# Optimization experiments

Measured on AMD Instinct MI355X. Metric: run time of the kernel, lower is better.

Reference implementation:

```python
import jax, jax.numpy as jnp
import numpy as np

NEG = -1e30  # safe 'log zero' for fp32 (avoids -inf NaNs in grads)


def _ctc_loss(logits, targets, input_lengths, target_lengths):
    """PyTorch-semantics CTC loss: blank=0, reduction='mean', zero_infinity=True.
    logits: [B,T,C] (pre-log-softmax), targets: [B,S] padded, lengths: [B].
    """
    B, T, C = logits.shape
    S = targets.shape[1]
    L = 2 * S + 1  # extended target length (blanks interleaved)
    logp = jax.nn.log_softmax(logits, axis=-1)  # [B,T,C]

    # extended targets: blank, y1, blank, y2, ..., blank
    ext = jnp.zeros((B, L), jnp.int32).at[:, 1::2].set(targets.astype(jnp.int32))
    lp_ext = jnp.take_along_axis(
        logp, jnp.broadcast_to(ext[:, None, :], (B, T, L)), axis=2)  # [B,T,L]

    pos = jnp.arange(L)
    ext_m2 = jnp.pad(ext, ((0, 0), (2, 0)))[:, :L]
    can_skip = (ext != 0) & (ext != ext_m2) & (pos >= 2)  # [B,L]

    def shift(a, k):
        return jnp.pad(a, ((0, 0), (k, 0)), constant_values=NEG)[:, :L]

    def lse3(a, b, c):
        m = jnp.maximum(jnp.maximum(a, b), c)
        return m + jnp.log(jnp.exp(a - m) + jnp.exp(b - m) + jnp.exp(c - m))

    alpha0 = (jnp.full((B, L), NEG, logits.dtype)
              .at[:, 0].set(lp_ext[:, 0, 0])
              .at[:, 1].set(lp_ext[:, 0, 1]))

    def step(alpha, xs):
        lp_t, t = xs  # lp_t: [B,L]
        a2 = shift(alpha, 1)
        a3 = jnp.where(can_skip, shift(alpha, 2), NEG)
        new = lp_t + lse3(alpha, a2, a3)
        # freeze alpha once past each sample's input_length
        alpha = jnp.where((t < input_lengths)[:, None], new, alpha)
        return alpha, None

    lp_T = jnp.swapaxes(lp_ext, 0, 1)  # [T,B,L]
    alpha, _ = jax.lax.scan(step, alpha0, (lp_T[1:], jnp.arange(1, T)))

    i1 = (2 * target_lengths - 1).astype(jnp.int32)
    i2 = (2 * target_lengths).astype(jnp.int32)
    a_last = jnp.take_along_axis(alpha, i1[:, None], axis=1)[:, 0]
    a_blank = jnp.take_along_axis(alpha, i2[:, None], axis=1)[:, 0]
    loss = -jnp.logaddexp(a_last, a_blank)  # [B]
    loss = jnp.where(loss > 1e29, 0.0, loss)  # zero_infinity=True
    return jnp.mean(loss / target_lengths.astype(loss.dtype))


def setup_inputs() -> dict:
    key = jax.random.key(0)
    ks = jax.random.split(key, 8)
    B, T = 32, 2000
    C_err, S_err = 4, 50
    C_ph, S_ph = 64, 200
    error_logits = jax.random.normal(ks[0], (B, T, C_err), jnp.float32)
    phoneme_logits = jax.random.normal(ks[1], (B, T, C_ph), jnp.float32)
    # labels in [1, C): blank=0 never appears in targets
    error_targets = jax.random.randint(ks[2], (B, S_err), 1, C_err, jnp.int32)
    phoneme_targets = jax.random.randint(ks[3], (B, S_ph), 1, C_ph, jnp.int32)
    error_input_lengths = jax.random.randint(ks[4], (B,), T - T // 4, T + 1, jnp.int32)
    phoneme_input_lengths = jax.random.randint(ks[5], (B,), T - T // 4, T + 1, jnp.int32)
    error_target_lengths = jax.random.randint(ks[6], (B,), S_err // 2, S_err + 1, jnp.int32)
    phoneme_target_lengths = jax.random.randint(ks[7], (B,), S_ph // 2, S_ph + 1, jnp.int32)
    return {
        "error_logits": error_logits,
        "phoneme_logits": phoneme_logits,
        "error_targets": error_targets,
        "phoneme_targets": phoneme_targets,
        "error_input_lengths": error_input_lengths,
        "phoneme_input_lengths": phoneme_input_lengths,
        "error_target_lengths": error_target_lengths,
        "phoneme_target_lengths": phoneme_target_lengths,
    }


def reference(error_logits, phoneme_logits, error_targets, phoneme_targets,
              error_input_lengths, phoneme_input_lengths,
              error_target_lengths, phoneme_target_lengths):
    error_weight = 1.0
    phoneme_weight = 1.0
    error_loss = _ctc_loss(error_logits, error_targets,
                           error_input_lengths, error_target_lengths)
    phoneme_loss = _ctc_loss(phoneme_logits, phoneme_targets,
                             phoneme_input_lengths, phoneme_target_lengths)
    total_loss = error_weight * error_loss + phoneme_weight * phoneme_loss
    return total_loss
```

## Files before the change

### kernel.cpp

```cpp
#include <hip/hip_runtime.h>
#include <math.h>


static constexpr float  LOG2E = 1.4426950408889634f;
static constexpr double LN2D  = 0.6931471805599453;
static constexpr int GROWS = 2032;

#define DPP_WAVE_SHR1   0x138
#define DPP_ROW_SHR(n)  (0x110 | (n))
#define DPP_ROW_BCAST15 0x142
#define DPP_ROW_BCAST31 0x143

__device__ __forceinline__ float fexp2(float x) {
  return __builtin_amdgcn_exp2f(x);
}
__device__ __forceinline__ float flog2(float x) {
  return __builtin_amdgcn_logf(x);
}

__device__ __forceinline__ double dpp_shr1_f64(double x) {
  int lo = __double2loint(x), hi = __double2hiint(x);
  lo = __builtin_amdgcn_update_dpp(0, lo, DPP_WAVE_SHR1, 0xf, 0xf, true);
  hi = __builtin_amdgcn_update_dpp(0, hi, DPP_WAVE_SHR1, 0xf, 0xf, true);
  return __hiloint2double(hi, lo);
}

__device__ __forceinline__ int imax2(int a, int b) { return a > b ? a : b; }

__device__ __forceinline__ int wave_imax(int v) {
  v = imax2(v, __builtin_amdgcn_update_dpp(0, v, DPP_ROW_SHR(1), 0xf, 0xf, true));
  v = imax2(v, __builtin_amdgcn_update_dpp(0, v, DPP_ROW_SHR(2), 0xf, 0xf, true));
  v = imax2(v, __builtin_amdgcn_update_dpp(0, v, DPP_ROW_SHR(4), 0xf, 0xf, true));
  v = imax2(v, __builtin_amdgcn_update_dpp(0, v, DPP_ROW_SHR(8), 0xf, 0xf, true));
  v = imax2(v, __builtin_amdgcn_update_dpp(0, v, DPP_ROW_BCAST15, 0xf, 0xf, true));
  v = imax2(v, __builtin_amdgcn_update_dpp(0, v, DPP_ROW_BCAST31, 0xf, 0xf, true));
  return __builtin_amdgcn_readlane(v, 63);
}

template <int SZ>
__device__ __forceinline__ void dma(const float* g, float* l) {
  auto gp = (const __attribute__((address_space(1))) void*)g;
  auto lp = (__attribute__((address_space(3))) void*)l;
  if constexpr (SZ == 4) {
    __builtin_amdgcn_global_load_lds(gp, lp, 4, 0, 0);
  } else {
    __builtin_amdgcn_global_load_lds(gp, lp, 16, 0, 0);
  }
}

__device__ __forceinline__ void wait_vmcnt16() {
  __builtin_amdgcn_sched_barrier(0);
  __builtin_amdgcn_s_waitcnt(20336);
  __builtin_amdgcn_sched_barrier(0);
}
__device__ __forceinline__ void wait_vmcnt0() {
  __builtin_amdgcn_sched_barrier(0);
  __builtin_amdgcn_s_waitcnt(3952);
  __builtin_amdgcn_sched_barrier(0);
}


__global__ __launch_bounds__(256) void gather_all_kernel(
    const float* __restrict__ ph_logits, const float* __restrict__ err_logits,
    const int* __restrict__ ph_tgt, const int* __restrict__ err_tgt,
    float* __restrict__ Gph, float* __restrict__ Ger,
    float* __restrict__ Lpb_ph, float* __restrict__ Lpb_er) {
  const int lane = threadIdx.x & 63;
  const int t = blockIdx.x * 4 + (threadIdx.x >> 6);
  const int b = blockIdx.y;
  if (blockIdx.z == 0) {
    const float z = ph_logits[((size_t)b * 2000 + t) * 64 + lane] * LOG2E;
    float m = z;
#pragma unroll
    for (int off = 32; off >= 1; off >>= 1) m = fmaxf(m, __shfl_xor(m, off, 64));
    const float zm = z - m;
    const float e = fexp2(zm);
    float s = e;
#pragma unroll
    for (int off = 32; off >= 1; off >>= 1) s += __shfl_xor(s, off, 64);
    const int ei = __float_as_int(e);
    const float e0 = __int_as_float(__builtin_amdgcn_readlane(ei, 0));
    const float inv0 = 1.0f / e0;
    const int* tb = ph_tgt + b * 200;
    float o[4];
#pragma unroll
    for (int k = 0; k < 4; ++k) {
      const int si = lane * 4 + k;
      const int cls = (si < 200) ? tb[si] : 0;
      const float v = __int_as_float(__builtin_amdgcn_ds_bpermute(cls << 2, ei));
      o[k] = (si < 200) ? (v * inv0) : 0.0f;
    }
    *(float4*)(Gph + ((size_t)b * GROWS + t) * 256 + lane * 4) =
        make_float4(o[0], o[1], o[2], o[3]);
    if (lane == 0)
      Lpb_ph[(size_t)b * GROWS + t] = zm - flog2(s);
  } else {
    const float4 v = *(const float4*)(err_logits + ((size_t)b * 2000 + t) * 4);
    const float z0 = v.x * LOG2E, z1 = v.y * LOG2E, z2 = v.z * LOG2E,
                z3 = v.w * LOG2E;
    const float m = fmaxf(fmaxf(z0, z1), fmaxf(z2, z3));
    const float e0 = fexp2(z0 - m), e1 = fexp2(z1 - m);
    const float e2 = fexp2(z2 - m), e3 = fexp2(z3 - m);
    const int c1 = err_tgt[b * 50 + (lane < 50 ? lane : 49)];
    const float num = (c1 == 1) ? e1 : (c1 == 2) ? e2 : e3;
    Ger[((size_t)b * GROWS + t) * 64 + lane] = (lane < 50) ? (num / e0) : 0.0f;
    if (lane == 0)
      Lpb_er[(size_t)b * GROWS + t] = (z0 - m) - flog2(e0 + e1 + e2 + e3);
  }
}

template <int P> struct RowP { float v[P]; };

template <int P>
__device__ __forceinline__ RowP<P> load_rowp(const float* p) {
  RowP<P> r;
  if constexpr (P == 4) {
    const float4 a = *(const float4*)p;
    r.v[0] = a.x; r.v[1] = a.y; r.v[2] = a.z; r.v[3] = a.w;
  } else {
    r.v[0] = *p;
  }
  return r;
}

template <int P>
__device__ __forceinline__ void bl_renorm(double (&B)[P], double (&L)[P],
                                          int& K) {
  double mm = B[0];
#pragma unroll
  for (int k = 0; k < P; ++k) mm = fmax(fmax(mm, B[k]), L[k]);
  const int ex = (__double2hiint(mm) >> 20) & 0x7ff;
  const int emax = wave_imax(ex);
  if (emax > 0) {
    int d = 1523 - emax;
    if (d > 1023) d = 1023;
    if (d < -1022) d = -1022;
    const double sc = __hiloint2double((d + 1023) << 20, 0);
#pragma unroll
    for (int k = 0; k < P; ++k) { B[k] *= sc; L[k] *= sc; }
    K += d;
  }
}

template <int P>
__device__ __forceinline__ void bl_step(double (&B)[P], double (&L)[P],
                                        const double (&skipm)[P],
                                        const RowP<P>& f) {
  const double Lm1 = dpp_shr1_f64(L[P - 1]);
  double nB[P], nL[P];
#pragma unroll
  for (int k = 0; k < P; ++k) {
    const double Lp = (k >= 1) ? L[k - 1] : Lm1;
    nB[k] = B[k] + Lp;
    nL[k] = (double)f.v[k] * fma(skipm[k], Lp, B[k] + L[k]);
  }
#pragma unroll
  for (int k = 0; k < P; ++k) { B[k] = nB[k]; L[k] = nL[k]; }
}

template <int P, int S>
__device__ __forceinline__ void chain_bl3(
    const float* __restrict__ Glab,
    const float* __restrict__ Lpb,
    const int* __restrict__ tb, int len, int tl,
    float* __restrict__ out, double* sa, float* stage) {
  constexpr int LSTRIDE = 64 * P;
  const int lane = threadIdx.x;

  float spb = 0.f;
  for (int t = lane; t < len; t += 64) spb += Lpb[t];
#pragma unroll
  for (int off = 32; off >= 1; off >>= 1) spb += __shfl_xor(spb, off, 64);

  double skipm[P];
#pragma unroll
  for (int k = 0; k < P; ++k) {
    const int s = lane * P + k;
    skipm[k] = (s >= 1 && s < S && tb[s] != tb[s - 1]) ? 1.0 : 0.0;
  }

  double B[P], L[P];
#pragma unroll
  for (int k = 0; k < P; ++k) { B[k] = 0.0; L[k] = 0.0; }
  {
    const float r0 = Glab[0];
    if (lane == 0) { B[0] = 1.0; L[0] = (double)r0; }
  }
  int K = 0;

  const int ngroups = (len - 1) / 16;
  auto issue_group = [&](int g, int buf) {
    const float* rb = Glab + (size_t)(1 + g * 16) * LSTRIDE + lane * P;
    float* lb = stage + (size_t)buf * 16 * LSTRIDE;
#pragma unroll
    for (int u = 0; u < 16; ++u)
      dma<P * 4>(rb + u * LSTRIDE, lb + u * LSTRIDE);
  };

  if (ngroups >= 1) issue_group(0, 0);
  if (ngroups >= 2) issue_group(1, 1);

  for (int g = 0; g < ngroups; ++g) {
    if (g + 1 < ngroups) wait_vmcnt16();
    else                 wait_vmcnt0();
    bl_renorm<P>(B, L, K);
    const float* lb = stage + (size_t)(g & 1) * 16 * LSTRIDE + lane * P;
    RowP<P> c0 = load_rowp<P>(lb);
    RowP<P> c1 = load_rowp<P>(lb + LSTRIDE);
#pragma unroll
    for (int u = 0; u < 16; ++u) {
      RowP<P> c2 = c1;
      if (u + 2 < 16) c2 = load_rowp<P>(lb + (u + 2) * LSTRIDE);
      bl_step<P>(B, L, skipm, c0);
      c0 = c1; c1 = c2;
    }
    if (g + 2 < ngroups) issue_group(g + 2, g & 1);
  }
  for (int t = 1 + ngroups * 16; t < len; ++t) {
    if (((t - 1) & 15) == 0) bl_renorm<P>(B, L, K);
    const RowP<P> f = load_rowp<P>(Glab + (size_t)t * LSTRIDE + lane * P);
    bl_step<P>(B, L, skipm, f);
  }

  double* saB = sa;
  double* saL = sa + 64 * P;
#pragma unroll
  for (int k = 0; k < P; ++k) {
    saB[lane * P + k] = B[k];
    saL[lane * P + k] = L[k];
  }
  __syncthreads();
  if (lane == 0) {
    const double a = saL[tl - 1] + saB[tl];
    float loss = (float)((double)K * LN2D - log(a) - (double)spb * LN2D);
    if (!(loss < 1e29f)) loss = 0.f;
    atomicAdd(out, loss / ((float)tl * 32.0f));
  }
}

__global__ __launch_bounds__(64) void ctc_chains_dma_kernel(
    const float* __restrict__ Gph, const float* __restrict__ Ger,
    const float* __restrict__ Lpb_ph, const float* __restrict__ Lpb_er,
    const int* __restrict__ err_tgt, const int* __restrict__ ph_tgt,
    const int* __restrict__ err_il, const int* __restrict__ ph_il,
    const int* __restrict__ err_tl, const int* __restrict__ ph_tl,
    float* __restrict__ out) {
  __shared__ float stage[2 * 16 * 256];
  __shared__ double sa[512];
  const int blk = blockIdx.x;
  if (blk < 32) {
    int len = err_il[blk]; if (len > 2000) len = 2000;
    chain_bl3<1, 50>(Ger + (size_t)blk * GROWS * 64,
                     Lpb_er + (size_t)blk * GROWS, err_tgt + blk * 50, len,
                     err_tl[blk], out, sa, stage);
  } else {
    const int b = blk - 32;
    int len = ph_il[b]; if (len > 2000) len = 2000;
    chain_bl3<4, 200>(Gph + (size_t)b * GROWS * 256,
                      Lpb_ph + (size_t)b * GROWS, ph_tgt + b * 200, len,
                      ph_tl[b], out, sa, stage);
  }
}


__global__ __launch_bounds__(256) void softmax4_kernel(
    const float* __restrict__ x, float* __restrict__ p, int nrows) {
  int r = blockIdx.x * blockDim.x + threadIdx.x;
  if (r >= nrows) return;
  float4 v = *reinterpret_cast<const float4*>(x + (size_t)r * 4);
  float z0 = v.x * LOG2E, z1 = v.y * LOG2E, z2 = v.z * LOG2E, z3 = v.w * LOG2E;
  float m = fmaxf(fmaxf(z0, z1), fmaxf(z2, z3));
  float e0 = fexp2(z0 - m), e1 = fexp2(z1 - m);
  float e2 = fexp2(z2 - m), e3 = fexp2(z3 - m);
  float inv = 1.0f / (e0 + e1 + e2 + e3);
  float4 o;
  o.x = e0 * inv; o.y = e1 * inv; o.z = e2 * inv; o.w = e3 * inv;
  *reinterpret_cast<float4*>(p + (size_t)r * 4) = o;
}

__global__ __launch_bounds__(256) void softmax64_kernel(
    const float* __restrict__ x, float* __restrict__ p, int nrows) {
  int row = blockIdx.x * 4 + (threadIdx.x >> 6);
  int lane = threadIdx.x & 63;
  if (row >= nrows) return;
  float z = x[(size_t)row * 64 + lane] * LOG2E;
  float m = z;
#pragma unroll
  for (int off = 32; off >= 1; off >>= 1) m = fmaxf(m, __shfl_xor(m, off, 64));
  float e = fexp2(z - m);
  float s = e;
#pragma unroll
  for (int off = 32; off >= 1; off >>= 1) s += __shfl_xor(s, off, 64);
  p[(size_t)row * 64 + lane] = e * (1.0f / s);
}

template <int C, int S, int R>
__device__ __forceinline__ void ctc_chain_lin_fb(
    const float* __restrict__ p_b, const int* __restrict__ tgt_b,
    int len, int tl, float* __restrict__ out, double* sa) {
  constexpr int L = 2 * S + 1;
  const int lane = threadIdx.x;
  int idx[R];
  double skipm[R];
#pragma unroll
  for (int j = 0; j < R; ++j) {
    const int l = lane * R + j;
    int cls = 0;
    bool sk = false;
    if (l & 1) {
      const int s = (l - 1) >> 1;
      const int sc = (s < S) ? s : (S - 1);
      cls = tgt_b[sc];
      if (s >= 1 && s < S) sk = (cls != tgt_b[s - 1]);
    }
    idx[j] = cls * 4;
    skipm[j] = sk ? 1.0 : 0.0;
  }
  double alpha[R];
#pragma unroll
  for (int j = 0; j < R; ++j) {
    const int l = lane * R + j;
    alpha[j] = (l <= 1) ? (double)p_b[idx[j] >> 2] : 0.0;
  }
  int K = 0;
  const int cl = lane & (C - 1);
  float rv = p_b[(size_t)((1 < len - 1) ? 1 : (len - 1)) * C + cl];
  float pf[R];
#pragma unroll
  for (int j = 0; j < R; ++j)
    pf[j] = __int_as_float(__builtin_amdgcn_ds_bpermute(idx[j], __float_as_int(rv)));
  rv = p_b[(size_t)((2 < len - 1) ? 2 : (len - 1)) * C + cl];
  for (int t = 1; t < len; ++t) {
    if ((t & 31) == 0) {
      double m = alpha[0];
#pragma unroll
      for (int j = 1; j < R; ++j) m = fmax(m, alpha[j]);
#pragma unroll
      for (int off = 1; off < 64; off <<= 1) m = fmax(m, __shfl_xor(m, off, 64));
      const long long bits = __double_as_longlong(m);
      const int e = (int)((bits >> 52) & 0x7FF);
      if (e > 0) {
        const double sc = __longlong_as_double((long long)(2046 - e) << 52);
#pragma unroll
        for (int j = 0; j < R; ++j) alpha[j] *= sc;
        K += 1023 - e;
      }
    }
    const int tn = (t + 2 < len) ? (t + 2) : (len - 1);
    const float rvn = p_b[(size_t)tn * C + cl];
    float pfn[R];
#pragma unroll
    for (int j = 0; j < R; ++j)
      pfn[j] = __int_as_float(__builtin_amdgcn_ds_bpermute(idx[j], __float_as_int(rv)));
    double am1 = __shfl_up(alpha[R - 1], 1, 64);
    double am2 = __shfl_up(alpha[R - 2], 1, 64);
    if (lane == 0) { am1 = 0.0; am2 = 0.0; }
    double na[R];
#pragma unroll
    for (int j = 0; j < R; ++j) {
      const double a0 = alpha[j];
      const double a1 = (j >= 1) ? alpha[j - 1] : am1;
      const double a2 = (j >= 2) ? alpha[j - 2] : ((j == 1) ? am1 : am2);
      double s = a0 + a1;
      s = fma(skipm[j], a2, s);
      na[j] = (double)pf[j] * s;
    }
#pragma unroll
    for (int j = 0; j < R; ++j) alpha[j] = na[j];
#pragma unroll
    for (int j = 0; j < R; ++j) pf[j] = pfn[j];
    rv = rvn;
  }
#pragma unroll
  for (int j = 0; j < R; ++j) {
    const int l = lane * R + j;
    if (l < L) sa[l] = alpha[j];
  }
  __syncthreads();
  if (lane == 0) {
    const double a = sa[2 * tl - 1] + sa[2 * tl];
    float loss = (float)((double)K * LN2D - log(a));
    if (!(loss < 1e29f)) loss = 0.0f;
    atomicAdd(out, loss / ((float)tl * 32.0f));
  }
}

__global__ __launch_bounds__(64) void ctc_chains_fb_kernel(
    const float* __restrict__ p_err, const float* __restrict__ p_ph,
    const int* __restrict__ err_tgt, const int* __restrict__ ph_tgt,
    const int* __restrict__ err_il, const int* __restrict__ ph_il,
    const int* __restrict__ err_tl, const int* __restrict__ ph_tl,
    float* __restrict__ out) {
  __shared__ double sa[512];
  const int T = 2000;
  const int blk = blockIdx.x;
  if (blk < 32) {
    const int b = blk;
    int len = err_il[b]; if (len > T) len = T;
    ctc_chain_lin_fb<4, 50, 2>(p_err + (size_t)b * T * 4, err_tgt + b * 50, len,
                               err_tl[b], out, sa);
  } else {
    const int b = blk - 32;
    int len = ph_il[b]; if (len > T) len = T;
    ctc_chain_lin_fb<64, 200, 7>(p_ph + (size_t)b * T * 64, ph_tgt + b * 200,
                                 len, ph_tl[b], out, sa);
  }
}


extern "C" void kernel_launch(void* const* d_in, const int* in_sizes, int n_in,
                              void* d_out, int out_size, void* d_ws,
                              size_t ws_size, hipStream_t stream) {
  const float* err_logits = (const float*)d_in[0];
  const float* ph_logits  = (const float*)d_in[1];
  const int* err_tgt = (const int*)d_in[2];
  const int* ph_tgt  = (const int*)d_in[3];
  const int* err_il  = (const int*)d_in[4];
  const int* ph_il   = (const int*)d_in[5];
  const int* err_tl  = (const int*)d_in[6];
  const int* ph_tl   = (const int*)d_in[7];
  float* out = (float*)d_out;

  const size_t gph = (size_t)32 * GROWS * 256;
  const size_t ger = (size_t)32 * GROWS * 64;
  const size_t lpb = (size_t)32 * GROWS;
  const size_t need = (gph + ger + 2 * lpb) * sizeof(float);

  (void)hipMemsetAsync(d_out, 0, sizeof(float), stream);

  if (ws_size >= need) {
    float* Gph = (float*)d_ws;
    float* Ger = Gph + gph;
    float* Lpb_ph = Ger + ger;
    float* Lpb_er = Lpb_ph + lpb;
    dim3 grid(500, 32, 2);
    gather_all_kernel<<<grid, 256, 0, stream>>>(ph_logits, err_logits, ph_tgt,
                                                err_tgt, Gph, Ger, Lpb_ph,
                                                Lpb_er);
    ctc_chains_dma_kernel<<<64, 64, 0, stream>>>(Gph, Ger, Lpb_ph, Lpb_er,
                                                 err_tgt, ph_tgt, err_il,
                                                 ph_il, err_tl, ph_tl, out);
  } else {
    const int B = 32, T = 2000;
    const int rows = B * T;
    float* p_err = (float*)d_ws;
    float* p_ph  = p_err + (size_t)rows * 4;
    softmax4_kernel<<<(rows + 255) / 256, 256, 0, stream>>>(err_logits, p_err, rows);
    softmax64_kernel<<<(rows + 3) / 4, 256, 0, stream>>>(ph_logits, p_ph, rows);
    ctc_chains_fb_kernel<<<64, 64, 0, stream>>>(p_err, p_ph, err_tgt, ph_tgt,
                                                err_il, ph_il, err_tl, ph_tl, out);
  }
}
```

Before: 229.6 us.

## Stream raw per-class exp rows and gather targets from LDS ring in chain kernel

The phoneme gather kernel now writes 64 per-class exp ratios (relative to class 0) per timestep instead of a pre-gathered 256-wide label row. The chain kernel DMAs these 64-float rows into a 2048-float LDS ring and does the target-class gather itself through indexed LDS reads. This cuts the intermediate buffer traffic and the DMA volume per step by about 4x, and frees LDS. In exchange each step does four scattered LDS reads that may bank-conflict, and it uses a deeper register prefetch.

New measurement: 277.7 us. 1.21x slower.

```diff
diff --git a/kernel.cpp b/kernel.cpp
--- a/kernel.cpp
+++ b/kernel.cpp
@@ -37,20 +37,15 @@
   return __builtin_amdgcn_readlane(v, 63);
 }
 
-template <int SZ>
-__device__ __forceinline__ void dma(const float* g, float* l) {
-  auto gp = (const __attribute__((address_space(1))) void*)g;
-  auto lp = (__attribute__((address_space(3))) void*)l;
-  if constexpr (SZ == 4) {
-    __builtin_amdgcn_global_load_lds(gp, lp, 4, 0, 0);
-  } else {
-    __builtin_amdgcn_global_load_lds(gp, lp, 16, 0, 0);
-  }
-}
-
-__device__ __forceinline__ void wait_vmcnt16() {
+__device__ __forceinline__ void dma4(const float* g, float* l) {
+  __builtin_amdgcn_global_load_lds((const __attribute__((address_space(1))) void*)g,
+                                   (__attribute__((address_space(3))) void*)l,
+                                   4, 0, 0);
+}
+
+__device__ __forceinline__ void wait_vmcnt12() {
   __builtin_amdgcn_sched_barrier(0);
-  __builtin_amdgcn_s_waitcnt(20336);
+  __builtin_amdgcn_s_waitcnt(3964);
   __builtin_amdgcn_sched_barrier(0);
 }
 __device__ __forceinline__ void wait_vmcnt0() {
@@ -69,31 +64,15 @@
   const int t = blockIdx.x * 4 + (threadIdx.x >> 6);
   const int b = blockIdx.y;
   if (blockIdx.z == 0) {
-    const float z = ph_logits[((size_t)b * 2000 + t) * 64 + lane] * LOG2E;
-    float m = z;
-#pragma unroll
-    for (int off = 32; off >= 1; off >>= 1) m = fmaxf(m, __shfl_xor(m, off, 64));
-    const float zm = z - m;
-    const float e = fexp2(zm);
-    float s = e;
+    const float z = ph_logits[((size_t)b * 2000 + t) * 64 + lane];
+    const float z0 =
+        __int_as_float(__builtin_amdgcn_readfirstlane(__float_as_int(z)));
+    const float r = fexp2((z - z0) * LOG2E);
+    float s = r;
 #pragma unroll
     for (int off = 32; off >= 1; off >>= 1) s += __shfl_xor(s, off, 64);
-    const int ei = __float_as_int(e);
-    const float e0 = __int_as_float(__builtin_amdgcn_readlane(ei, 0));
-    const float inv0 = 1.0f / e0;
-    const int* tb = ph_tgt + b * 200;
-    float o[4];
-#pragma unroll
-    for (int k = 0; k < 4; ++k) {
-      const int si = lane * 4 + k;
-      const int cls = (si < 200) ? tb[si] : 0;
-      const float v = __int_as_float(__builtin_amdgcn_ds_bpermute(cls << 2, ei));
-      o[k] = (si < 200) ? (v * inv0) : 0.0f;
-    }
-    *(float4*)(Gph + ((size_t)b * GROWS + t) * 256 + lane * 4) =
-        make_float4(o[0], o[1], o[2], o[3]);
-    if (lane == 0)
-      Lpb_ph[(size_t)b * GROWS + t] = zm - flog2(s);
+    Gph[((size_t)b * GROWS + t) * 64 + lane] = r;
+    if (lane == 0) Lpb_ph[(size_t)b * GROWS + t] = -flog2(s);
   } else {
     const float4 v = *(const float4*)(err_logits + ((size_t)b * 2000 + t) * 4);
     const float z0 = v.x * LOG2E, z1 = v.y * LOG2E, z2 = v.z * LOG2E,
@@ -112,18 +91,6 @@
 template <int P> struct RowP { float v[P]; };
 
 template <int P>
-__device__ __forceinline__ RowP<P> load_rowp(const float* p) {
-  RowP<P> r;
-  if constexpr (P == 4) {
-    const float4 a = *(const float4*)p;
-    r.v[0] = a.x; r.v[1] = a.y; r.v[2] = a.z; r.v[3] = a.w;
-  } else {
-    r.v[0] = *p;
-  }
-  return r;
-}
-
-template <int P>
 __device__ __forceinline__ void bl_renorm(double (&B)[P], double (&L)[P],
                                           int& K) {
   double mm = B[0];
@@ -158,13 +125,26 @@
   for (int k = 0; k < P; ++k) { B[k] = nB[k]; L[k] = nL[k]; }
 }
 
-template <int P, int S>
-__device__ __forceinline__ void chain_bl3(
+template <int P, bool RAW>
+__device__ __forceinline__ RowP<P> gread(const float* ring, int rowf,
+                                         const int (&clsf)[P],
+                                         const float (&maskv)[P]) {
+  RowP<P> r;
+#pragma unroll
+  for (int k = 0; k < P; ++k) {
+    float v = ring[rowf + clsf[k]];
+    if constexpr (RAW) v *= maskv[k];
+    r.v[k] = v;
+  }
+  return r;
+}
+
+template <int P, int S, bool RAW>
+__device__ __forceinline__ void chain_bl4(
     const float* __restrict__ Glab,
     const float* __restrict__ Lpb,
     const int* __restrict__ tb, int len, int tl,
-    float* __restrict__ out, double* sa, float* stage) {
-  constexpr int LSTRIDE = 64 * P;
+    float* __restrict__ out, double* sa, float* ring) {
   const int lane = threadIdx.x;
 
   float spb = 0.f;
@@ -173,52 +153,69 @@
   for (int off = 32; off >= 1; off >>= 1) spb += __shfl_xor(spb, off, 64);
 
   double skipm[P];
+  int clsf[P];
+  float maskv[P];
 #pragma unroll
   for (int k = 0; k < P; ++k) {
     const int s = lane * P + k;
     skipm[k] = (s >= 1 && s < S && tb[s] != tb[s - 1]) ? 1.0 : 0.0;
+    if constexpr (RAW) {
+      clsf[k] = (s < S) ? tb[s] : 0;
+      maskv[k] = (s < S) ? 1.0f : 0.0f;
+    } else {
+      clsf[k] = lane * P + k;
+      maskv[k] = 1.0f;
+    }
   }
 
   double B[P], L[P];
 #pragma unroll
   for (int k = 0; k < P; ++k) { B[k] = 0.0; L[k] = 0.0; }
   {
-    const float r0 = Glab[0];
+    const float r0 = Glab[RAW ? tb[0] : 0];
     if (lane == 0) { B[0] = 1.0; L[0] = (double)r0; }
   }
   int K = 0;
 
   const int ngroups = (len - 1) / 16;
-  auto issue_group = [&](int g, int buf) {
-    const float* rb = Glab + (size_t)(1 + g * 16) * LSTRIDE + lane * P;
-    float* lb = stage + (size_t)buf * 16 * LSTRIDE;
-#pragma unroll
-    for (int u = 0; u < 16; ++u)
-      dma<P * 4>(rb + u * LSTRIDE, lb + u * LSTRIDE);
+  auto issue_group = [&](int g) {
+    const float* rb = Glab + (size_t)(1 + g * 16) * 64 + lane;
+    float* lb = ring + ((g & 1) * 16) * 64;
+#pragma unroll
+    for (int u = 0; u < 16; ++u) dma4(rb + u * 64, lb + u * 64);
   };
 
-  if (ngroups >= 1) issue_group(0, 0);
-  if (ngroups >= 2) issue_group(1, 1);
-
+  if (ngroups >= 1) issue_group(0);
+  if (ngroups >= 2) issue_group(1);
+
+  RowP<P> c0, c1, c2, c3;
+  int rowf = 0;
   for (int g = 0; g < ngroups; ++g) {
-    if (g + 1 < ngroups) wait_vmcnt16();
+    if (g + 1 < ngroups) wait_vmcnt12();
     else                 wait_vmcnt0();
     bl_renorm<P>(B, L, K);
-    const float* lb = stage + (size_t)(g & 1) * 16 * LSTRIDE + lane * P;
-    RowP<P> c0 = load_rowp<P>(lb);
-    RowP<P> c1 = load_rowp<P>(lb + LSTRIDE);
+    if (g == 0) {
+      c0 = gread<P, RAW>(ring, 0, clsf, maskv);
+      c1 = gread<P, RAW>(ring, 64, clsf, maskv);
+      c2 = gread<P, RAW>(ring, 128, clsf, maskv);
+      c3 = gread<P, RAW>(ring, 192, clsf, maskv);
+      rowf = 256;
+    }
 #pragma unroll
     for (int u = 0; u < 16; ++u) {
-      RowP<P> c2 = c1;
-      if (u + 2 < 16) c2 = load_rowp<P>(lb + (u + 2) * LSTRIDE);
+      const RowP<P> cn = gread<P, RAW>(ring, rowf, clsf, maskv);
+      rowf = (rowf + 64) & 2047;
       bl_step<P>(B, L, skipm, c0);
-      c0 = c1; c1 = c2;
-    }
-    if (g + 2 < ngroups) issue_group(g + 2, g & 1);
+      c0 = c1; c1 = c2; c2 = c3; c3 = cn;
+    }
+    if (g + 2 < ngroups) issue_group(g + 2);
   }
   for (int t = 1 + ngroups * 16; t < len; ++t) {
     if (((t - 1) & 15) == 0) bl_renorm<P>(B, L, K);
-    const RowP<P> f = load_rowp<P>(Glab + (size_t)t * LSTRIDE + lane * P);
+    RowP<P> f;
+#pragma unroll
+    for (int k = 0; k < P; ++k)
+      f.v[k] = Glab[(size_t)t * 64 + clsf[k]] * maskv[k];
     bl_step<P>(B, L, skipm, f);
   }
 
@@ -238,27 +235,27 @@
   }
 }
 
-__global__ __launch_bounds__(64) void ctc_chains_dma_kernel(
+__global__ __launch_bounds__(64) void ctc_chains_raw_kernel(
     const float* __restrict__ Gph, const float* __restrict__ Ger,
     const float* __restrict__ Lpb_ph, const float* __restrict__ Lpb_er,
     const int* __restrict__ err_tgt, const int* __restrict__ ph_tgt,
     const int* __restrict__ err_il, const int* __restrict__ ph_il,
     const int* __restrict__ err_tl, const int* __restrict__ ph_tl,
     float* __restrict__ out) {
-  __shared__ float stage[2 * 16 * 256];
+  __shared__ float ring[2048];
   __shared__ double sa[512];
   const int blk = blockIdx.x;
   if (blk < 32) {
     int len = err_il[blk]; if (len > 2000) len = 2000;
-    chain_bl3<1, 50>(Ger + (size_t)blk * GROWS * 64,
-                     Lpb_er + (size_t)blk * GROWS, err_tgt + blk * 50, len,
-                     err_tl[blk], out, sa, stage);
+    chain_bl4<1, 50, false>(Ger + (size_t)blk * GROWS * 64,
+                            Lpb_er + (size_t)blk * GROWS, err_tgt + blk * 50,
+                            len, err_tl[blk], out, sa, ring);
   } else {
     const int b = blk - 32;
     int len = ph_il[b]; if (len > 2000) len = 2000;
-    chain_bl3<4, 200>(Gph + (size_t)b * GROWS * 256,
-                      Lpb_ph + (size_t)b * GROWS, ph_tgt + b * 200, len,
-                      ph_tl[b], out, sa, stage);
+    chain_bl4<4, 200, true>(Gph + (size_t)b * GROWS * 64,
+                            Lpb_ph + (size_t)b * GROWS, ph_tgt + b * 200, len,
+                            ph_tl[b], out, sa, ring);
   }
 }
 
@@ -421,7 +418,7 @@
   const int* ph_tl   = (const int*)d_in[7];
   float* out = (float*)d_out;
 
-  const size_t gph = (size_t)32 * GROWS * 256;
+  const size_t gph = (size_t)32 * GROWS * 64;
   const size_t ger = (size_t)32 * GROWS * 64;
   const size_t lpb = (size_t)32 * GROWS;
   const size_t need = (gph + ger + 2 * lpb) * sizeof(float);
@@ -437,7 +434,7 @@
     gather_all_kernel<<<grid, 256, 0, stream>>>(ph_logits, err_logits, ph_tgt,
                                                 err_tgt, Gph, Ger, Lpb_ph,
                                                 Lpb_er);
-    ctc_chains_dma_kernel<<<64, 64, 0, stream>>>(Gph, Ger, Lpb_ph, Lpb_er,
+    ctc_chains_raw_kernel<<<64, 64, 0, stream>>>(Gph, Ger, Lpb_ph, Lpb_er,
                                                  err_tgt, ph_tgt, err_il,
                                                  ph_il, err_tl, ph_tl, out);
   } else {
```

## Split CTC alpha recursion across two waves with pipelined boundary exchange

Applied to the files above, without the earlier changes.

The phoneme chain's extended-state axis is split between two wavefronts per block, with two states per lane instead of four. Wave 0 runs the first half one 16-step window ahead and writes its last column's values and scale exponent to shared memory. Wave 1 then consumes those boundary values one window later, rescaled to its own exponent. DMA staging becomes a 4-slot ring, and the final log-likelihood combines the two halves' separate scale factors. The aim is to shorten the serial dependency chain per step, at the cost of a block barrier every 16 steps and more complex scaling logic.

Result: slower. 276.5 us (+20.4%).

```diff
diff --git a/kernel.cpp b/kernel.cpp
--- a/kernel.cpp
+++ b/kernel.cpp
@@ -37,15 +37,15 @@
   return __builtin_amdgcn_readlane(v, 63);
 }
 
-template <int SZ>
-__device__ __forceinline__ void dma(const float* g, float* l) {
-  auto gp = (const __attribute__((address_space(1))) void*)g;
-  auto lp = (__attribute__((address_space(3))) void*)l;
-  if constexpr (SZ == 4) {
-    __builtin_amdgcn_global_load_lds(gp, lp, 4, 0, 0);
-  } else {
-    __builtin_amdgcn_global_load_lds(gp, lp, 16, 0, 0);
-  }
+__device__ __forceinline__ void dma4(const float* g, float* l) {
+  __builtin_amdgcn_global_load_lds((const __attribute__((address_space(1))) void*)g,
+                                   (__attribute__((address_space(3))) void*)l,
+                                   4, 0, 0);
+}
+__device__ __forceinline__ void dma16(const float* g, float* l) {
+  __builtin_amdgcn_global_load_lds((const __attribute__((address_space(1))) void*)g,
+                                   (__attribute__((address_space(3))) void*)l,
+                                   16, 0, 0);
 }
 
 __device__ __forceinline__ void wait_vmcnt16() {
@@ -109,14 +109,16 @@
   }
 }
 
+
 template <int P> struct RowP { float v[P]; };
 
 template <int P>
-__device__ __forceinline__ RowP<P> load_rowp(const float* p) {
+__device__ __forceinline__ RowP<P> lread(const float* p) {
   RowP<P> r;
-  if constexpr (P == 4) {
-    const float4 a = *(const float4*)p;
-    r.v[0] = a.x; r.v[1] = a.y; r.v[2] = a.z; r.v[3] = a.w;
+  if constexpr (P == 2) {
+    const float2 a = *(const float2*)p;
+    r.v[0] = a.x;
+    r.v[1] = a.y;
   } else {
     r.v[0] = *p;
   }
@@ -124,8 +126,8 @@
 }
 
 template <int P>
-__device__ __forceinline__ void bl_renorm(double (&B)[P], double (&L)[P],
-                                          int& K) {
+__device__ __forceinline__ int bl_renorm(double (&B)[P], double (&L)[P],
+                                         int& K) {
   double mm = B[0];
 #pragma unroll
   for (int k = 0; k < P; ++k) mm = fmax(fmax(mm, B[k]), L[k]);
@@ -140,13 +142,16 @@
     for (int k = 0; k < P; ++k) { B[k] *= sc; L[k] *= sc; }
     K += d;
   }
+  return emax;
 }
 
 template <int P>
 __device__ __forceinline__ void bl_step(double (&B)[P], double (&L)[P],
                                         const double (&skipm)[P],
-                                        const RowP<P>& f) {
-  const double Lm1 = dpp_shr1_f64(L[P - 1]);
+                                        const RowP<P>& f, double bndv,
+                                        int lane) {
+  double Lm1 = dpp_shr1_f64(L[P - 1]);
+  if (lane == 0) Lm1 = bndv;
   double nB[P], nL[P];
 #pragma unroll
   for (int k = 0; k < P; ++k) {
@@ -158,107 +163,196 @@
   for (int k = 0; k < P; ++k) { B[k] = nB[k]; L[k] = nL[k]; }
 }
 
-template <int P, int S>
-__device__ __forceinline__ void chain_bl3(
-    const float* __restrict__ Glab,
+template <int P, int S, int RSF, bool PH>
+__device__ __forceinline__ void split_chain(
+    const float* __restrict__ G,
     const float* __restrict__ Lpb,
-    const int* __restrict__ tb, int len, int tl,
-    float* __restrict__ out, double* sa, float* stage) {
-  constexpr int LSTRIDE = 64 * P;
-  const int lane = threadIdx.x;
+    const int* __restrict__ tb, int len, int tl, float* __restrict__ out,
+    float* ring, double* bnd, int* kexs, double* saB, double* saL,
+    int* kfin) {
+  constexpr int SLOT = 16 * RSF;
+  constexpr int HALF = 64 * P;
+  constexpr bool BDEAD = (HALF >= S + 1);
+  const int wid = threadIdx.x >> 6;
+  const int lane = threadIdx.x & 63;
+  const int off = wid ? HALF : 0;
 
   float spb = 0.f;
-  for (int t = lane; t < len; t += 64) spb += Lpb[t];
-#pragma unroll
-  for (int off = 32; off >= 1; off >>= 1) spb += __shfl_xor(spb, off, 64);
-
-  double skipm[P];
+  if (wid == 0) {
+    for (int t = lane; t < len; t += 64) spb += Lpb[t];
+#pragma unroll
+    for (int o = 32; o >= 1; o >>= 1) spb += __shfl_xor(spb, o, 64);
+  }
+
+  double skipm[P], B[P], L[P];
 #pragma unroll
   for (int k = 0; k < P; ++k) {
-    const int s = lane * P + k;
+    const int s = off + lane * P + k;
     skipm[k] = (s >= 1 && s < S && tb[s] != tb[s - 1]) ? 1.0 : 0.0;
-  }
-
-  double B[P], L[P];
-#pragma unroll
-  for (int k = 0; k < P; ++k) { B[k] = 0.0; L[k] = 0.0; }
-  {
-    const float r0 = Glab[0];
-    if (lane == 0) { B[0] = 1.0; L[0] = (double)r0; }
+    B[k] = 0.0;
+    L[k] = 0.0;
   }
   int K = 0;
-
-  const int ngroups = (len - 1) / 16;
-  auto issue_group = [&](int g, int buf) {
-    const float* rb = Glab + (size_t)(1 + g * 16) * LSTRIDE + lane * P;
-    float* lb = stage + (size_t)buf * 16 * LSTRIDE;
-#pragma unroll
-    for (int u = 0; u < 16; ++u)
-      dma<P * 4>(rb + u * LSTRIDE, lb + u * LSTRIDE);
+  if (wid == 0 && lane == 0) {
+    B[0] = 1.0;
+    L[0] = (double)G[0];
+  }
+
+  const int ntot = (len - 1 + 15) >> 4;
+
+  auto issue = [&](int w) {
+    const float* rb = G + (size_t)(1 + w * 16) * RSF + lane * (PH ? 4 : 1);
+    float* lb = ring + (w & 3) * SLOT;
+#pragma unroll
+    for (int u = 0; u < 16; ++u) {
+      if constexpr (PH) dma16(rb + u * RSF, lb + u * RSF);
+      else              dma4(rb + u * RSF, lb + u * RSF);
+    }
   };
 
-  if (ngroups >= 1) issue_group(0, 0);
-  if (ngroups >= 2) issue_group(1, 1);
-
-  for (int g = 0; g < ngroups; ++g) {
-    if (g + 1 < ngroups) wait_vmcnt16();
-    else                 wait_vmcnt0();
-    bl_renorm<P>(B, L, K);
-    const float* lb = stage + (size_t)(g & 1) * 16 * LSTRIDE + lane * P;
-    RowP<P> c0 = load_rowp<P>(lb);
-    RowP<P> c1 = load_rowp<P>(lb + LSTRIDE);
-#pragma unroll
-    for (int u = 0; u < 16; ++u) {
-      RowP<P> c2 = c1;
-      if (u + 2 < 16) c2 = load_rowp<P>(lb + (u + 2) * LSTRIDE);
-      bl_step<P>(B, L, skipm, c0);
-      c0 = c1; c1 = c2;
-    }
-    if (g + 2 < ngroups) issue_group(g + 2, g & 1);
-  }
-  for (int t = 1 + ngroups * 16; t < len; ++t) {
-    if (((t - 1) & 15) == 0) bl_renorm<P>(B, L, K);
-    const RowP<P> f = load_rowp<P>(Glab + (size_t)t * LSTRIDE + lane * P);
-    bl_step<P>(B, L, skipm, f);
-  }
-
-  double* saB = sa;
-  double* saL = sa + 64 * P;
+  if (wid == 0) {
+    if (ntot > 0) issue(0);
+    if (ntot > 1) issue(1);
+  }
+
+  for (int p = 0; p <= ntot; ++p) {
+    if (wid == 0) {
+      if (p < ntot) {
+        if (p + 1 < ntot) wait_vmcnt16();
+        else              wait_vmcnt0();
+        bl_renorm<P>(B, L, K);
+        if (lane == 0) kexs[p & 1] = K;
+        const int cnt = (len - 1 - p * 16 < 16) ? (len - 1 - p * 16) : 16;
+        const float* lb = ring + (p & 3) * SLOT + lane * P;
+        const int bb = (p & 1) * 16;
+        if (cnt == 16) {
+          RowP<P> c0 = lread<P>(lb);
+          RowP<P> c1 = lread<P>(lb + RSF);
+          RowP<P> c2 = lread<P>(lb + 2 * RSF);
+          RowP<P> c3 = lread<P>(lb + 3 * RSF);
+#pragma unroll
+          for (int u = 0; u < 16; ++u) {
+            RowP<P> cn = c3;
+            if (u + 4 < 16) cn = lread<P>(lb + (u + 4) * RSF);
+            if constexpr (!BDEAD)
+              if (lane == 63) bnd[bb + u] = L[P - 1];
+            bl_step<P>(B, L, skipm, c0, 0.0, lane);
+            c0 = c1; c1 = c2; c2 = c3; c3 = cn;
+          }
+        } else {
+          for (int u = 0; u < cnt; ++u) {
+            const RowP<P> f = lread<P>(lb + u * RSF);
+            if constexpr (!BDEAD)
+              if (lane == 63) bnd[bb + u] = L[P - 1];
+            bl_step<P>(B, L, skipm, f, 0.0, lane);
+          }
+        }
+        if (p + 2 < ntot) issue(p + 2);
+      }
+    } else if constexpr (!BDEAD) {
+      if (p >= 1) {
+        const int w = p - 1;
+        const int emaxB = bl_renorm<P>(B, L, K);
+        const int kA = kexs[w & 1];
+        double adj;
+        if (emaxB == 0) {
+          K = kA;
+          adj = 1.0;
+        } else {
+          int d = K - kA;
+          if (d > 1022) d = 1022;
+          if (d < -1022) d = -1022;
+          adj = __hiloint2double((d + 1023) << 20, 0);
+        }
+        double bv = 0.0;
+        if (lane < 16) bv = bnd[(w & 1) * 16 + lane];
+        const int bvlo = __double2loint(bv), bvhi = __double2hiint(bv);
+        const int cnt = (len - 1 - w * 16 < 16) ? (len - 1 - w * 16) : 16;
+        const float* lb = ring + (w & 3) * SLOT + HALF + lane * P;
+        if (cnt == 16) {
+          RowP<P> c0 = lread<P>(lb);
+          RowP<P> c1 = lread<P>(lb + RSF);
+          RowP<P> c2 = lread<P>(lb + 2 * RSF);
+          RowP<P> c3 = lread<P>(lb + 3 * RSF);
+#pragma unroll
+          for (int u = 0; u < 16; ++u) {
+            RowP<P> cn = c3;
+            if (u + 4 < 16) cn = lread<P>(lb + (u + 4) * RSF);
+            const double bndv =
+                __hiloint2double(__builtin_amdgcn_readlane(bvhi, u),
+                                 __builtin_amdgcn_readlane(bvlo, u)) * adj;
+            bl_step<P>(B, L, skipm, c0, bndv, lane);
+            c0 = c1; c1 = c2; c2 = c3; c3 = cn;
+          }
+        } else {
+          for (int u = 0; u < cnt; ++u) {
+            const RowP<P> f = lread<P>(lb + u * RSF);
+            const double bndv =
+                __hiloint2double(__builtin_amdgcn_readlane(bvhi, u),
+                                 __builtin_amdgcn_readlane(bvlo, u)) * adj;
+            bl_step<P>(B, L, skipm, f, bndv, lane);
+          }
+        }
+      }
+    }
+    __syncthreads();
+  }
+
 #pragma unroll
   for (int k = 0; k < P; ++k) {
-    saB[lane * P + k] = B[k];
-    saL[lane * P + k] = L[k];
-  }
+    saB[off + lane * P + k] = B[k];
+    saL[off + lane * P + k] = L[k];
+  }
+  if (lane == 0) kfin[wid] = K;
   __syncthreads();
-  if (lane == 0) {
-    const double a = saL[tl - 1] + saB[tl];
-    float loss = (float)((double)K * LN2D - log(a) - (double)spb * LN2D);
-    if (!(loss < 1e29f)) loss = 0.f;
+  if (wid == 0 && lane == 0) {
+    const int i1 = tl - 1, i2 = tl;
+    const double Lv = saL[i1], Bv = saB[i2];
+    const double K1 = (double)((i1 < HALF) ? kfin[0] : kfin[1]);
+    const double K2 = (double)((i2 < HALF) ? kfin[0] : kfin[1]);
+    const double u1 = log(Lv) - K1 * LN2D;
+    const double u2 = log(Bv) - K2 * LN2D;
+    const double mx = fmax(u1, u2);
+    float loss;
+    if (mx < -1e300) {
+      loss = 0.f;
+    } else {
+      const double lse = mx + log(exp(u1 - mx) + exp(u2 - mx));
+      loss = (float)(-lse - (double)spb * LN2D);
+      if (!(loss < 1e29f)) loss = 0.f;
+    }
     atomicAdd(out, loss / ((float)tl * 32.0f));
   }
 }
 
-__global__ __launch_bounds__(64) void ctc_chains_dma_kernel(
+__global__ __launch_bounds__(128) void ctc_chains_split_kernel(
     const float* __restrict__ Gph, const float* __restrict__ Ger,
     const float* __restrict__ Lpb_ph, const float* __restrict__ Lpb_er,
     const int* __restrict__ err_tgt, const int* __restrict__ ph_tgt,
     const int* __restrict__ err_il, const int* __restrict__ ph_il,
     const int* __restrict__ err_tl, const int* __restrict__ ph_tl,
     float* __restrict__ out) {
-  __shared__ float stage[2 * 16 * 256];
-  __shared__ double sa[512];
+  __shared__ float ring[4 * 16 * 256];
+  __shared__ double bnd[32];
+  __shared__ int kexs[2];
+  __shared__ double saB[256], saL[256];
+  __shared__ int kfin[2];
   const int blk = blockIdx.x;
   if (blk < 32) {
-    int len = err_il[blk]; if (len > 2000) len = 2000;
-    chain_bl3<1, 50>(Ger + (size_t)blk * GROWS * 64,
-                     Lpb_er + (size_t)blk * GROWS, err_tgt + blk * 50, len,
-                     err_tl[blk], out, sa, stage);
+    int len = err_il[blk];
+    if (len > 2000) len = 2000;
+    split_chain<1, 50, 64, false>(Ger + (size_t)blk * GROWS * 64,
+                                  Lpb_er + (size_t)blk * GROWS,
+                                  err_tgt + blk * 50, len, err_tl[blk], out,
+                                  ring, bnd, kexs, saB, saL, kfin);
   } else {
     const int b = blk - 32;
-    int len = ph_il[b]; if (len > 2000) len = 2000;
-    chain_bl3<4, 200>(Gph + (size_t)b * GROWS * 256,
-                      Lpb_ph + (size_t)b * GROWS, ph_tgt + b * 200, len,
-                      ph_tl[b], out, sa, stage);
+    int len = ph_il[b];
+    if (len > 2000) len = 2000;
+    split_chain<2, 200, 256, true>(Gph + (size_t)b * GROWS * 256,
+                                   Lpb_ph + (size_t)b * GROWS,
+                                   ph_tgt + b * 200, len, ph_tl[b], out, ring,
+                                   bnd, kexs, saB, saL, kfin);
   }
 }
 
@@ -437,9 +531,9 @@
     gather_all_kernel<<<grid, 256, 0, stream>>>(ph_logits, err_logits, ph_tgt,
                                                 err_tgt, Gph, Ger, Lpb_ph,
                                                 Lpb_er);
-    ctc_chains_dma_kernel<<<64, 64, 0, stream>>>(Gph, Ger, Lpb_ph, Lpb_er,
-                                                 err_tgt, ph_tgt, err_il,
-                                                 ph_il, err_tl, ph_tl, out);
+    ctc_chains_split_kernel<<<64, 128, 0, stream>>>(Gph, Ger, Lpb_ph, Lpb_er,
+                                                    err_tgt, ph_tgt, err_il,
+                                                    ph_il, err_tl, ph_tl, out);
   } else {
     const int B = 32, T = 2000;
     const int rows = B * T;
```
